# Performance work log

Hardware: AMD Instinct MI355X
Metric: run time of the kernel (lower is better)

The kernel has to match this reference:

```python
import jax, jax.numpy as jnp
import numpy as np

# --- static config (matches init_kwargs) ---
B, N, M = 128, 32, 32
C_IMG, NUM_HIDDEN, NUM_CLASSES = 1, 16, 3
INPUT_DIM = C_IMG + NUM_HIDDEN + NUM_CLASSES          # 20
OUT_DIM = NUM_HIDDEN + NUM_CLASSES + 2                # 21 (moving -> 2 action channels)
C_STATE = INPUT_DIM - C_IMG                           # 19
N_NEO, M_NEO = N - 2, M - 2                           # size_neo=None -> N-2
N_ACTIVE, M_ACTIVE = N - 2, M - 2
ITERATIONS = 10
IN_FEAT = 9 * INPUT_DIM + 2                           # 182, position='current'
THRESH = 0.0007


def setup_inputs() -> dict:
    key = jax.random.key(0)
    ks = jax.random.split(key, 7)
    images = jax.random.uniform(ks[0], (B, N, M, C_IMG), dtype=jnp.float32)
    W1 = jax.random.normal(ks[1], (IN_FEAT, 30), dtype=jnp.float32) * 0.08
    b1 = jnp.zeros((30,), jnp.float32)
    W2 = jax.random.normal(ks[2], (30, 30), dtype=jnp.float32) * 0.18
    b2 = jnp.zeros((30,), jnp.float32)
    W3 = jax.random.normal(ks[3], (30, OUT_DIM), dtype=jnp.float32) * 0.18
    b3 = jnp.zeros((OUT_DIM,), jnp.float32)
    return {"images": images, "W1": W1, "b1": b1, "W2": W2, "b2": b2, "W3": W3, "b3": b3}


def _custom_round(a):
    # positive -> +1, negative -> -1 (with deadzone |a| <= 0.0007 -> 0)
    return jnp.where(a > THRESH, 1, jnp.where(a < -THRESH, -1, 0)).astype(jnp.int32)


def _run(images, W1, b1, W2, b2, W3, b3):
    dx = jnp.arange(3)
    b_idx = jnp.arange(B)[:, None, None, None, None]        # (B,1,1,1,1)
    # fixed 3x3 windows into state (comms): state[x:x+3, y:y+3]
    sr = (jnp.arange(N_NEO)[:, None] + dx)[:, None, :, None]  # (Nn,1,3,1)
    sc = (jnp.arange(M_NEO)[:, None] + dx)[None, :, None, :]  # (1,Mn,1,3)
    half_n = N // 2
    half_m = M // 2

    # initial perception matrix: identity grid (N_neo == N_active)
    gx, gy = jnp.meshgrid(jnp.arange(N_NEO), jnp.arange(M_NEO), indexing="ij")
    perc0 = jnp.broadcast_to(jnp.stack([gx, gy], -1).astype(jnp.int32), (B, N_NEO, M_NEO, 2))
    state0 = jnp.zeros((B, N, M, C_STATE), jnp.float32)
    guesses0 = jnp.zeros((B * N_NEO * M_NEO, OUT_DIM), jnp.float32)

    def step(carry, _):
        state, perc, _ = carry
        px = perc[..., 0]  # (B,Nn,Mn) int32
        py = perc[..., 1]
        # dynamic 3x3 image patches at (px, py)
        rows = px[..., None, None] + dx[:, None]            # (B,Nn,Mn,3,1)
        cols = py[..., None, None] + dx[None, :]            # (B,Nn,Mn,1,3)
        perc_patch = images[b_idx, rows, cols, :]           # (B,Nn,Mn,3,3,C_IMG)
        comms = state[:, sr, sc, :]                          # (B,Nn,Mn,3,3,C_STATE)
        feat = jnp.concatenate([perc_patch, comms], axis=-1)  # (B,Nn,Mn,3,3,INPUT_DIM)
        feat = feat.reshape(B * N_NEO * M_NEO, 9 * INPUT_DIM)
        # position='current' features
        pos_x = ((px - half_n) / half_n).astype(jnp.float32).reshape(-1, 1)
        pos_y = ((py - half_m) / half_m).astype(jnp.float32).reshape(-1, 1)
        inp = jnp.concatenate([feat, pos_x, pos_y], axis=-1)  # (B*Nn*Mn, 182)
        h = jax.nn.relu(inp @ W1 + b1)
        h = jax.nn.relu(h @ W2 + b2)
        guesses = h @ W3 + b3                                 # (B*Nn*Mn, 21)
        outputs = guesses.reshape(B, N_NEO, M_NEO, OUT_DIM)
        state = state.at[:, 1:1 + N_NEO, 1:1 + M_NEO, :].add(outputs[..., :C_STATE])
        # movement: round actions to {-1,0,1}, add, clip to [0, N_active-1]
        delta = _custom_round(outputs[..., -2:])
        perc = jnp.clip(perc + delta, 0, N_ACTIVE - 1)
        return (state, perc, guesses), None

    (state, perc, guesses), _ = jax.lax.scan(step, (state0, perc0, guesses0), None, length=ITERATIONS)
    class_state = state[:, 1:1 + N_NEO, 1:1 + M_NEO, -NUM_CLASSES:]
    return class_state, guesses


def reference(images, W1, b1, W2, b2, W3, b3):
    return _run(images, W1, b1, W2, b2, W3, b3)
```

## Files before the change

### kernel.cpp

```cpp
#include <hip/hip_runtime.h>

#define B_      128
#define NPIX    32
#define NNEO    30
#define NCH     19
#define PLANE   1024
#define SROWS   10
#define SPLANE  (SROWS * NPIX)
#define OUTD    21
#define ITERS   10
#define THRESHV 0.0007f
#define HSTRIDE 31

#define STATE_ELEMS (B_ * NCH * PLANE)
#define NCELLS      (B_ * NNEO * NNEO)
#define CLASS_ELEMS (NCELLS * 3)


__global__ void nca_init(float* __restrict__ stateA, float* __restrict__ stateB) {
    int idx = blockIdx.x * blockDim.x + threadIdx.x;
    const int total = B_ * 124 * NCH;
    if (idx >= total) return;
    int c  = idx % NCH;
    int t2 = idx / NCH;
    int cellp = t2 % 124;
    int b    = t2 / 124;
    int i, j;
    if (cellp < 32)      { i = 0;  j = cellp; }
    else if (cellp < 64) { i = 31; j = cellp - 32; }
    else { int k = cellp - 64; i = 1 + (k >> 1); j = (k & 1) ? 31 : 0; }
    size_t off = ((size_t)(b * NCH + c)) * PLANE + i * NPIX + j;
    stateA[off] = 0.0f;
    stateB[off] = 0.0f;
}

#define ROW15(A, x, wrp) do { const float xx_ = (x); \
    const float* __restrict__ w_ = (wrp); \
    _Pragma("unroll") for (int o_ = 0; o_ < 15; o_++) (A)[o_] += xx_ * w_[o_]; \
} while (0)

#define ROW12(A, x, wrp) do { const float xx_ = (x); \
    const float* __restrict__ w_ = (wrp); \
    _Pragma("unroll") for (int o_ = 0; o_ < 12; o_++) (A)[o_] += xx_ * w_[o_]; \
} while (0)

#define ROW9(A, x, wrp) do { const float xx_ = (x); \
    const float* __restrict__ w_ = (wrp); \
    _Pragma("unroll") for (int o_ = 0; o_ < 9; o_++) (A)[o_] += xx_ * w_[o_]; \
} while (0)

template<int MODE>
__global__ __launch_bounds__(512, 4)
void nca_step(const float* __restrict__ img,
              const float* __restrict__ W1, const float* __restrict__ b1,
              const float* __restrict__ W2, const float* __restrict__ b2,
              const float* __restrict__ W3, const float* __restrict__ b3,
              const float* __restrict__ state_old, float* __restrict__ state_new,
              int* perc, float* __restrict__ guesses_out,
              float* __restrict__ class_out)
{
    __shared__ float s_state[NCH * SPLANE];
    __shared__ float s_img[NPIX * NPIX];
    __shared__ float s_h[256 * HSTRIDE];

    const int b   = blockIdx.y;
    const int rg  = blockIdx.x;
    const int i0  = rg * 8;
    const int nr  = (rg == 3) ? 6 : 8;
    const int tid = threadIdx.x;
    const int h   = __builtin_amdgcn_readfirstlane(tid >> 8);
    const int cell = tid & 255;
    const int qoff = h * 15;

    if (MODE != 0) {
        const float4* __restrict__ g4 = (const float4*)
            (state_old + (size_t)b * (NCH * PLANE) + i0 * NPIX);
        float4* s4 = (float4*)s_state;
        if (nr == 8) {
            for (int t = tid; t < NCH * 80; t += 512) {
                const int ch = t / 80, rem = t - ch * 80;
                s4[ch * 80 + rem] = g4[ch * 256 + rem];
            }
        } else {
            for (int t = tid; t < NCH * 64; t += 512) {
                const int ch = t / 64, rem = t - ch * 64;
                s4[ch * 80 + rem] = g4[ch * 256 + rem];
            }
        }
    }
    if (tid < 256)
        ((float4*)s_img)[tid] = ((const float4*)(img + (size_t)b * PLANE))[tid];
    __syncthreads();

    const int cells = nr * NNEO;
    const bool active = cell < cells;

    int r = 0, j = 0, i = 0, gcell = 0, px = 0, py = 0;
    if (active) {
        r = cell / NNEO;
        j = cell - r * NNEO;
        i = i0 + r;
        gcell = (b * NNEO + i) * NNEO + j;
        if (MODE == 0) { px = i; py = j; }
        else           { px = perc[2 * gcell]; py = perc[2 * gcell + 1]; }
    }

    float a1[15];
    {
        float acc[15];
#pragma unroll
        for (int o = 0; o < 15; o++) acc[o] = b1[qoff + o];
        if (active) {
            if (MODE == 0) {
#pragma clang loop unroll(disable)
                for (int pr = 0; pr < 3; pr++) {
#pragma clang loop unroll(disable)
                    for (int pc = 0; pc < 3; pc++) {
                        const float iv = s_img[(px + pr) * NPIX + (py + pc)];
                        ROW15(acc, iv, W1 + (pr * 3 + pc) * 600 + qoff);
                    }
                }
            } else {
#pragma clang loop unroll(disable)
                for (int pr = 0; pr < 3; pr++) {
#pragma clang loop unroll(disable)
                    for (int pc = 0; pc < 3; pc++) {
                        const float iv = s_img[(px + pr) * NPIX + (py + pc)];
                        const float* __restrict__ wp =
                            W1 + (pr * 3 + pc) * 600 + qoff;
                        const int soff = (r + pr) * NPIX + (j + pc);
                        float fv[NCH];
#pragma unroll
                        for (int ch = 0; ch < NCH; ch++)
                            fv[ch] = s_state[ch * SPLANE + soff];
                        ROW15(acc, iv, wp);
#pragma unroll
                        for (int ch = 0; ch < NCH; ch++)
                            ROW15(acc, fv[ch], wp + (ch + 1) * 30);
                    }
                }
            }
            const float posx = (float)(px - 16) * 0.0625f;
            const float posy = (float)(py - 16) * 0.0625f;
            ROW15(acc, posx, W1 + 180 * 30 + qoff);
            ROW15(acc, posy, W1 + 181 * 30 + qoff);
        }
#pragma unroll
        for (int o = 0; o < 15; o++) a1[o] = fmaxf(acc[o], 0.0f);
        if (active) {
#pragma unroll
            for (int o = 0; o < 15; o++) s_h[cell * HSTRIDE + qoff + o] = a1[o];
        }
    }
    __syncthreads();

    float h2[15];
    {
        float acc[15];
#pragma unroll
        for (int o = 0; o < 15; o++) acc[o] = b2[qoff + o];
        if (active) {
            if (h == 0) {
#pragma unroll
                for (int k = 0; k < 15; k++)
                    ROW15(acc, a1[k], W2 + k * 30);
#pragma clang loop unroll(disable)
                for (int k = 15; k < 30; k++) {
                    const float x = s_h[cell * HSTRIDE + k];
                    ROW15(acc, x, W2 + k * 30);
                }
            } else {
#pragma clang loop unroll(disable)
                for (int k = 0; k < 15; k++) {
                    const float x = s_h[cell * HSTRIDE + k];
                    ROW15(acc, x, W2 + k * 30 + 15);
                }
#pragma unroll
                for (int k = 0; k < 15; k++)
                    ROW15(acc, a1[k], W2 + (k + 15) * 30 + 15);
            }
        }
#pragma unroll
        for (int o = 0; o < 15; o++) h2[o] = fmaxf(acc[o], 0.0f);
    }
    __syncthreads();
    if (active) {
#pragma unroll
        for (int o = 0; o < 15; o++) s_h[cell * HSTRIDE + qoff + o] = h2[o];
    }
    __syncthreads();

    if (active) {
        const int cen  = (i + 1) * NPIX + (j + 1);
        const int lcen = (r + 1) * NPIX + (j + 1);
        float* __restrict__ snp =
            state_new + (size_t)b * (NCH * PLANE) + cen;
        if (h == 0) {
            float ov[12];
#pragma unroll
            for (int c = 0; c < 12; c++) ov[c] = b3[c];
#pragma unroll
            for (int k = 0; k < 15; k++)
                ROW12(ov, h2[k], W3 + k * 21);
#pragma clang loop unroll(disable)
            for (int k = 15; k < 30; k++) {
                const float x = s_h[cell * HSTRIDE + k];
                ROW12(ov, x, W3 + k * 21);
            }
            if (MODE == 2) {
                float* __restrict__ g = guesses_out + (size_t)gcell * OUTD;
#pragma unroll
                for (int c = 0; c < 12; c++) g[c] = ov[c];
            } else if (MODE == 0) {
#pragma unroll
                for (int c = 0; c < 12; c++) snp[c * PLANE] = ov[c];
            } else {
#pragma unroll
                for (int c = 0; c < 12; c++)
                    snp[c * PLANE] = s_state[c * SPLANE + lcen] + ov[c];
            }
        } else {
            float ov[9];
#pragma unroll
            for (int c = 0; c < 9; c++) ov[c] = b3[12 + c];
#pragma clang loop unroll(disable)
            for (int k = 0; k < 15; k++) {
                const float x = s_h[cell * HSTRIDE + k];
                ROW9(ov, x, W3 + k * 21 + 12);
            }
#pragma unroll
            for (int k = 0; k < 15; k++)
                ROW9(ov, h2[k], W3 + (k + 15) * 21 + 12);
            if (MODE == 2) {
                float* __restrict__ g = guesses_out + (size_t)gcell * OUTD;
#pragma unroll
                for (int c = 0; c < 9; c++) g[12 + c] = ov[c];
                float* __restrict__ cs = class_out + (size_t)gcell * 3;
#pragma unroll
                for (int cc = 0; cc < 3; cc++)
                    cs[cc] = s_state[(16 + cc) * SPLANE + lcen] + ov[4 + cc];
            } else {
                if (MODE == 0) {
#pragma unroll
                    for (int c = 0; c < 7; c++) snp[(12 + c) * PLANE] = ov[c];
                } else {
#pragma unroll
                    for (int c = 0; c < 7; c++)
                        snp[(12 + c) * PLANE] =
                            s_state[(12 + c) * SPLANE + lcen] + ov[c];
                }
                int dxm = (ov[7] > THRESHV) ? 1 : ((ov[7] < -THRESHV) ? -1 : 0);
                int dym = (ov[8] > THRESHV) ? 1 : ((ov[8] < -THRESHV) ? -1 : 0);
                px += dxm; py += dym;
                px = (px < 0) ? 0 : ((px > NNEO - 1) ? NNEO - 1 : px);
                py = (py < 0) ? 0 : ((py > NNEO - 1) ? NNEO - 1 : py);
                perc[2 * gcell + 0] = px;
                perc[2 * gcell + 1] = py;
            }
        }
    }
}

extern "C" void kernel_launch(void* const* d_in, const int* in_sizes, int n_in,
                              void* d_out, int out_size, void* d_ws, size_t ws_size,
                              hipStream_t stream) {
    const float* img = (const float*)d_in[0];
    const float* W1  = (const float*)d_in[1];
    const float* b1  = (const float*)d_in[2];
    const float* W2  = (const float*)d_in[3];
    const float* b2  = (const float*)d_in[4];
    const float* W3  = (const float*)d_in[5];
    const float* b3  = (const float*)d_in[6];

    float* out = (float*)d_out;
    float* class_out   = out;
    float* guesses_out = out + CLASS_ELEMS;

    float* stateA = (float*)d_ws;
    float* stateB = stateA + STATE_ELEMS;
    int*   perc   = (int*)(stateB + STATE_ELEMS);

    {
        const int total = B_ * 124 * NCH;
        nca_init<<<(total + 255) / 256, 256, 0, stream>>>(stateA, stateB);
    }

    const dim3 grid(4, B_);
    nca_step<0><<<grid, 512, 0, stream>>>(img, W1, b1, W2, b2, W3, b3,
                                          stateA, stateB, perc,
                                          guesses_out, class_out);
    for (int t = 1; t < ITERS - 1; t++) {
        const float* so = (t & 1) ? stateB : stateA;
        float*       sn = (t & 1) ? stateA : stateB;
        nca_step<1><<<grid, 512, 0, stream>>>(img, W1, b1, W2, b2, W3, b3,
                                              so, sn, perc,
                                              guesses_out, class_out);
    }
    nca_step<2><<<grid, 512, 0, stream>>>(img, W1, b1, W2, b2, W3, b3,
                                          stateB, stateA, perc,
                                          guesses_out, class_out);
}
```

Baseline: 382.5 us.

## Split hidden units across four thread groups per cell with 1024-thread blocks

Each cell is now handled by four thread groups instead of two. Each group computes 8 first-layer and 8 second-layer hidden units over overlapping ranges, plus a 6-wide slice of the output. Blocks grow to 1024 threads and the row split changes to 8,8,7,7. This halves per-thread FMA chains and register pressure to expose more parallelism, at the cost of redundantly computing overlapping hidden units and more shared-memory traffic for the full 30-wide reads in layers 2 and 3.

```diff
diff --git a/kernel.cpp b/kernel.cpp
--- a/kernel.cpp
+++ b/kernel.cpp
@@ -34,23 +34,18 @@
     stateB[off] = 0.0f;
 }
 
-#define ROW15(A, x, wrp) do { const float xx_ = (x); \
+#define ROW8(A, x, wrp) do { const float xx_ = (x); \
     const float* __restrict__ w_ = (wrp); \
-    _Pragma("unroll") for (int o_ = 0; o_ < 15; o_++) (A)[o_] += xx_ * w_[o_]; \
+    _Pragma("unroll") for (int o_ = 0; o_ < 8; o_++) (A)[o_] += xx_ * w_[o_]; \
 } while (0)
 
-#define ROW12(A, x, wrp) do { const float xx_ = (x); \
+#define ROW6(A, x, wrp) do { const float xx_ = (x); \
     const float* __restrict__ w_ = (wrp); \
-    _Pragma("unroll") for (int o_ = 0; o_ < 12; o_++) (A)[o_] += xx_ * w_[o_]; \
+    _Pragma("unroll") for (int o_ = 0; o_ < 6; o_++) (A)[o_] += xx_ * w_[o_]; \
 } while (0)
 
-#define ROW9(A, x, wrp) do { const float xx_ = (x); \
-    const float* __restrict__ w_ = (wrp); \
-    _Pragma("unroll") for (int o_ = 0; o_ < 9; o_++) (A)[o_] += xx_ * w_[o_]; \
-} while (0)
-
 template<int MODE>
-__global__ __launch_bounds__(512, 4)
+__global__ __launch_bounds__(1024, 8)
 void nca_step(const float* __restrict__ img,
               const float* __restrict__ W1, const float* __restrict__ b1,
               const float* __restrict__ W2, const float* __restrict__ b2,
@@ -65,25 +60,26 @@
 
     const int b   = blockIdx.y;
     const int rg  = blockIdx.x;
-    const int i0  = rg * 8;
-    const int nr  = (rg == 3) ? 6 : 8;
+    const int i0  = (rg < 2) ? rg * 8 : 16 + (rg - 2) * 7;
+    const int nr  = (rg < 2) ? 8 : 7;
     const int tid = threadIdx.x;
-    const int h   = __builtin_amdgcn_readfirstlane(tid >> 8);
+    const int qh  = __builtin_amdgcn_readfirstlane(tid >> 8);
     const int cell = tid & 255;
-    const int qoff = h * 15;
+    const int qoff = (qh == 0) ? 0 : (qh == 1) ? 8 : (qh == 2) ? 14 : 22;
+    const int off3 = 5 * qh;
 
     if (MODE != 0) {
         const float4* __restrict__ g4 = (const float4*)
             (state_old + (size_t)b * (NCH * PLANE) + i0 * NPIX);
         float4* s4 = (float4*)s_state;
         if (nr == 8) {
-            for (int t = tid; t < NCH * 80; t += 512) {
+            for (int t = tid; t < NCH * 80; t += 1024) {
                 const int ch = t / 80, rem = t - ch * 80;
                 s4[ch * 80 + rem] = g4[ch * 256 + rem];
             }
         } else {
-            for (int t = tid; t < NCH * 64; t += 512) {
-                const int ch = t / 64, rem = t - ch * 64;
+            for (int t = tid; t < NCH * 72; t += 1024) {
+                const int ch = t / 72, rem = t - ch * 72;
                 s4[ch * 80 + rem] = g4[ch * 256 + rem];
             }
         }
@@ -105,152 +101,132 @@
         else           { px = perc[2 * gcell]; py = perc[2 * gcell + 1]; }
     }
 
-    float a1[15];
-    {
-        float acc[15];
-#pragma unroll
-        for (int o = 0; o < 15; o++) acc[o] = b1[qoff + o];
-        if (active) {
-            if (MODE == 0) {
-#pragma clang loop unroll(disable)
-                for (int pr = 0; pr < 3; pr++) {
-#pragma clang loop unroll(disable)
-                    for (int pc = 0; pc < 3; pc++) {
-                        const float iv = s_img[(px + pr) * NPIX + (py + pc)];
-                        ROW15(acc, iv, W1 + (pr * 3 + pc) * 600 + qoff);
-                    }
-                }
-            } else {
-#pragma clang loop unroll(disable)
-                for (int pr = 0; pr < 3; pr++) {
-#pragma clang loop unroll(disable)
-                    for (int pc = 0; pc < 3; pc++) {
-                        const float iv = s_img[(px + pr) * NPIX + (py + pc)];
-                        const float* __restrict__ wp =
-                            W1 + (pr * 3 + pc) * 600 + qoff;
-                        const int soff = (r + pr) * NPIX + (j + pc);
-                        float fv[NCH];
-#pragma unroll
-                        for (int ch = 0; ch < NCH; ch++)
-                            fv[ch] = s_state[ch * SPLANE + soff];
-                        ROW15(acc, iv, wp);
-#pragma unroll
-                        for (int ch = 0; ch < NCH; ch++)
-                            ROW15(acc, fv[ch], wp + (ch + 1) * 30);
-                    }
-                }
-            }
-            const float posx = (float)(px - 16) * 0.0625f;
-            const float posy = (float)(py - 16) * 0.0625f;
-            ROW15(acc, posx, W1 + 180 * 30 + qoff);
-            ROW15(acc, posy, W1 + 181 * 30 + qoff);
-        }
-#pragma unroll
-        for (int o = 0; o < 15; o++) a1[o] = fmaxf(acc[o], 0.0f);
-        if (active) {
-#pragma unroll
-            for (int o = 0; o < 15; o++) s_h[cell * HSTRIDE + qoff + o] = a1[o];
-        }
-    }
-    __syncthreads();
-
-    float h2[15];
-    {
-        float acc[15];
-#pragma unroll
-        for (int o = 0; o < 15; o++) acc[o] = b2[qoff + o];
-        if (active) {
-            if (h == 0) {
-#pragma unroll
-                for (int k = 0; k < 15; k++)
-                    ROW15(acc, a1[k], W2 + k * 30);
-#pragma clang loop unroll(disable)
-                for (int k = 15; k < 30; k++) {
-                    const float x = s_h[cell * HSTRIDE + k];
-                    ROW15(acc, x, W2 + k * 30);
-                }
-            } else {
-#pragma clang loop unroll(disable)
-                for (int k = 0; k < 15; k++) {
-                    const float x = s_h[cell * HSTRIDE + k];
-                    ROW15(acc, x, W2 + k * 30 + 15);
-                }
-#pragma unroll
-                for (int k = 0; k < 15; k++)
-                    ROW15(acc, a1[k], W2 + (k + 15) * 30 + 15);
-            }
-        }
-#pragma unroll
-        for (int o = 0; o < 15; o++) h2[o] = fmaxf(acc[o], 0.0f);
-    }
-    __syncthreads();
-    if (active) {
-#pragma unroll
-        for (int o = 0; o < 15; o++) s_h[cell * HSTRIDE + qoff + o] = h2[o];
-    }
-    __syncthreads();
-
-    if (active) {
+    float h1[8];
+#pragma unroll
+    for (int q = 0; q < 8; q++) h1[q] = b1[qoff + q];
+    if (active) {
+        if (MODE == 0) {
+#pragma clang loop unroll(disable)
+            for (int pr = 0; pr < 3; pr++) {
+#pragma clang loop unroll(disable)
+                for (int pc = 0; pc < 3; pc++) {
+                    const float iv = s_img[(px + pr) * NPIX + (py + pc)];
+                    ROW8(h1, iv, W1 + (pr * 3 + pc) * 600 + qoff);
+                }
+            }
+        } else {
+#pragma clang loop unroll(disable)
+            for (int pr = 0; pr < 3; pr++) {
+#pragma clang loop unroll(disable)
+                for (int pc = 0; pc < 3; pc++) {
+                    const float iv = s_img[(px + pr) * NPIX + (py + pc)];
+                    const float* __restrict__ wp =
+                        W1 + (pr * 3 + pc) * 600 + qoff;
+                    const int sb = (r + pr) * NPIX + (j + pc);
+                    float fv[NCH];
+#pragma unroll
+                    for (int ch = 0; ch < NCH; ch++)
+                        fv[ch] = s_state[ch * SPLANE + sb];
+                    ROW8(h1, iv, wp);
+#pragma unroll
+                    for (int ch = 0; ch < NCH; ch++)
+                        ROW8(h1, fv[ch], wp + (ch + 1) * 30);
+                }
+            }
+        }
+        const float posx = (float)(px - 16) * 0.0625f;
+        const float posy = (float)(py - 16) * 0.0625f;
+        ROW8(h1, posx, W1 + 180 * 30 + qoff);
+        ROW8(h1, posy, W1 + 181 * 30 + qoff);
+#pragma unroll
+        for (int q = 0; q < 8; q++) h1[q] = fmaxf(h1[q], 0.0f);
+#pragma unroll
+        for (int q = 0; q < 8; q++) s_h[cell * HSTRIDE + qoff + q] = h1[q];
+    }
+    __syncthreads();
+
+    float h2[8];
+#pragma unroll
+    for (int q = 0; q < 8; q++) h2[q] = b2[qoff + q];
+    if (active) {
+#pragma clang loop unroll(disable)
+        for (int k = 0; k < 30; k++) {
+            const float x = s_h[cell * HSTRIDE + k];
+            ROW8(h2, x, W2 + k * 30 + qoff);
+        }
+#pragma unroll
+        for (int q = 0; q < 8; q++) h2[q] = fmaxf(h2[q], 0.0f);
+    }
+    __syncthreads();
+    if (active) {
+#pragma unroll
+        for (int q = 0; q < 8; q++) s_h[cell * HSTRIDE + qoff + q] = h2[q];
+    }
+    __syncthreads();
+
+    float o[6];
+#pragma unroll
+    for (int c = 0; c < 6; c++) o[c] = b3[off3 + c];
+    if (active) {
+#pragma clang loop unroll(disable)
+        for (int k = 0; k < 30; k++) {
+            const float x = s_h[cell * HSTRIDE + k];
+            ROW6(o, x, W3 + k * 21 + off3);
+        }
+
         const int cen  = (i + 1) * NPIX + (j + 1);
         const int lcen = (r + 1) * NPIX + (j + 1);
-        float* __restrict__ snp =
-            state_new + (size_t)b * (NCH * PLANE) + cen;
-        if (h == 0) {
-            float ov[12];
-#pragma unroll
-            for (int c = 0; c < 12; c++) ov[c] = b3[c];
-#pragma unroll
-            for (int k = 0; k < 15; k++)
-                ROW12(ov, h2[k], W3 + k * 21);
-#pragma clang loop unroll(disable)
-            for (int k = 15; k < 30; k++) {
-                const float x = s_h[cell * HSTRIDE + k];
-                ROW12(ov, x, W3 + k * 21);
-            }
-            if (MODE == 2) {
-                float* __restrict__ g = guesses_out + (size_t)gcell * OUTD;
-#pragma unroll
-                for (int c = 0; c < 12; c++) g[c] = ov[c];
-            } else if (MODE == 0) {
-#pragma unroll
-                for (int c = 0; c < 12; c++) snp[c * PLANE] = ov[c];
+        if (MODE == 2) {
+            float* __restrict__ g = guesses_out + (size_t)gcell * OUTD;
+            if (qh == 0) {
+#pragma unroll
+                for (int c = 0; c < 6; c++) g[c] = o[c];
             } else {
 #pragma unroll
-                for (int c = 0; c < 12; c++)
-                    snp[c * PLANE] = s_state[c * SPLANE + lcen] + ov[c];
+                for (int c = 1; c < 6; c++) g[off3 + c] = o[c];
+            }
+            if (qh == 3) {
+                float* __restrict__ cs = class_out + (size_t)gcell * 3;
+#pragma unroll
+                for (int cc = 0; cc < 3; cc++)
+                    cs[cc] = s_state[(16 + cc) * SPLANE + lcen] + o[1 + cc];
             }
         } else {
-            float ov[9];
-#pragma unroll
-            for (int c = 0; c < 9; c++) ov[c] = b3[12 + c];
-#pragma clang loop unroll(disable)
-            for (int k = 0; k < 15; k++) {
-                const float x = s_h[cell * HSTRIDE + k];
-                ROW9(ov, x, W3 + k * 21 + 12);
-            }
-#pragma unroll
-            for (int k = 0; k < 15; k++)
-                ROW9(ov, h2[k], W3 + (k + 15) * 21 + 12);
-            if (MODE == 2) {
-                float* __restrict__ g = guesses_out + (size_t)gcell * OUTD;
-#pragma unroll
-                for (int c = 0; c < 9; c++) g[12 + c] = ov[c];
-                float* __restrict__ cs = class_out + (size_t)gcell * 3;
-#pragma unroll
-                for (int cc = 0; cc < 3; cc++)
-                    cs[cc] = s_state[(16 + cc) * SPLANE + lcen] + ov[4 + cc];
+            float* __restrict__ snp =
+                state_new + (size_t)b * (NCH * PLANE) + cen;
+            if (qh == 0) {
+#pragma unroll
+                for (int c = 0; c < 6; c++) {
+                    const float old =
+                        (MODE == 0) ? 0.0f : s_state[c * SPLANE + lcen];
+                    snp[c * PLANE] = old + o[c];
+                }
+            } else if (qh == 1) {
+#pragma unroll
+                for (int c = 1; c < 6; c++) {
+                    const int ch = 5 + c;
+                    const float old =
+                        (MODE == 0) ? 0.0f : s_state[ch * SPLANE + lcen];
+                    snp[ch * PLANE] = old + o[c];
+                }
+            } else if (qh == 2) {
+#pragma unroll
+                for (int c = 1; c < 6; c++) {
+                    const int ch = 10 + c;
+                    const float old =
+                        (MODE == 0) ? 0.0f : s_state[ch * SPLANE + lcen];
+                    snp[ch * PLANE] = old + o[c];
+                }
             } else {
-                if (MODE == 0) {
-#pragma unroll
-                    for (int c = 0; c < 7; c++) snp[(12 + c) * PLANE] = ov[c];
-                } else {
-#pragma unroll
-                    for (int c = 0; c < 7; c++)
-                        snp[(12 + c) * PLANE] =
-                            s_state[(12 + c) * SPLANE + lcen] + ov[c];
-                }
-                int dxm = (ov[7] > THRESHV) ? 1 : ((ov[7] < -THRESHV) ? -1 : 0);
-                int dym = (ov[8] > THRESHV) ? 1 : ((ov[8] < -THRESHV) ? -1 : 0);
+#pragma unroll
+                for (int c = 1; c < 4; c++) {
+                    const int ch = 15 + c;
+                    const float old =
+                        (MODE == 0) ? 0.0f : s_state[ch * SPLANE + lcen];
+                    snp[ch * PLANE] = old + o[c];
+                }
+                int dxm = (o[4] > THRESHV) ? 1 : ((o[4] < -THRESHV) ? -1 : 0);
+                int dym = (o[5] > THRESHV) ? 1 : ((o[5] < -THRESHV) ? -1 : 0);
                 px += dxm; py += dym;
                 px = (px < 0) ? 0 : ((px > NNEO - 1) ? NNEO - 1 : px);
                 py = (py < 0) ? 0 : ((py > NNEO - 1) ? NNEO - 1 : py);
@@ -286,17 +262,17 @@
     }
 
     const dim3 grid(4, B_);
-    nca_step<0><<<grid, 512, 0, stream>>>(img, W1, b1, W2, b2, W3, b3,
-                                          stateA, stateB, perc,
-                                          guesses_out, class_out);
+    nca_step<0><<<grid, 1024, 0, stream>>>(img, W1, b1, W2, b2, W3, b3,
+                                           stateA, stateB, perc,
+                                           guesses_out, class_out);
     for (int t = 1; t < ITERS - 1; t++) {
         const float* so = (t & 1) ? stateB : stateA;
         float*       sn = (t & 1) ? stateA : stateB;
-        nca_step<1><<<grid, 512, 0, stream>>>(img, W1, b1, W2, b2, W3, b3,
-                                              so, sn, perc,
-                                              guesses_out, class_out);
-    }
-    nca_step<2><<<grid, 512, 0, stream>>>(img, W1, b1, W2, b2, W3, b3,
-                                          stateB, stateA, perc,
-                                          guesses_out, class_out);
+        nca_step<1><<<grid, 1024, 0, stream>>>(img, W1, b1, W2, b2, W3, b3,
+                                               so, sn, perc,
+                                               guesses_out, class_out);
+    }
+    nca_step<2><<<grid, 1024, 0, stream>>>(img, W1, b1, W2, b2, W3, b3,
+                                           stateB, stateA, perc,
+                                           guesses_out, class_out);
 }
```

Result: slower. 394.8 us (+3.2%).
